# Optimization experiments

Hardware: AMD Instinct MI355X
Metric: run time of the kernel (lower is better)

The kernel has to match this reference:

```python
import jax, jax.numpy as jnp
import numpy as np

B, N, C, P, K = 8, 65536, 96, 96, 512


def _ln(x, g, b, eps=1e-5):
    mu = x.mean(axis=-1, keepdims=True)
    var = ((x - mu) ** 2).mean(axis=-1, keepdims=True)
    return (x - mu) * jax.lax.rsqrt(var + eps) * g + b


def setup_inputs():
    key = jax.random.key(0)
    ks = jax.random.split(key, 8)
    inp = {
        "pts_feat": jax.random.normal(ks[0], (B, N, C), jnp.float32),
        "sp_idx": jax.random.randint(ks[1], (B, N), 0, K, jnp.int64),
        "all_xyz": jax.random.normal(ks[2], (B, N, 3), jnp.float32),
        # pts_proj1: Linear(3,P) -> LN -> ReLU -> Linear(P,P) -> LN
        "W1": jax.random.normal(ks[3], (3, P), jnp.float32) / np.sqrt(3.0),
        "b1": jnp.zeros((P,), jnp.float32),
        "g1": jnp.ones((P,), jnp.float32),
        "be1": jnp.zeros((P,), jnp.float32),
        "W2": jax.random.normal(ks[4], (P, P), jnp.float32) / np.sqrt(P),
        "b2": jnp.zeros((P,), jnp.float32),
        "g2": jnp.ones((P,), jnp.float32),
        "be2": jnp.zeros((P,), jnp.float32),
        # pts_proj2: Linear(2P,P) -> LN -> ReLU -> Linear(P,1,no bias) -> Sigmoid
        "W3": jax.random.normal(ks[5], (2 * P, P), jnp.float32) / np.sqrt(2.0 * P),
        "b3": jnp.zeros((P,), jnp.float32),
        "g3": jnp.ones((P,), jnp.float32),
        "be3": jnp.zeros((P,), jnp.float32),
        "W4": jax.random.normal(ks[6], (P, 1), jnp.float32) / np.sqrt(P),
        "num_sp": K,
    }
    return inp


def reference(pts_feat, sp_idx, all_xyz, W1, b1, g1, be1, W2, b2, g2, be2,
              W3, b3, g3, be3, W4, num_sp):
    Bx, Nx, Cx = pts_feat.shape
    S = Bx * num_sp  # total superpoints across batch (uniform K per batch)
    idx = (sp_idx + jnp.arange(Bx, dtype=sp_idx.dtype)[:, None] * num_sp).reshape(-1)
    xyz = all_xyz.reshape(-1, 3)
    feat = pts_feat.reshape(-1, Cx)

    # scatter_norm: unit-sphere normalize per segment
    mn = jax.ops.segment_min(xyz, idx, num_segments=S)
    mx = jax.ops.segment_max(xyz, idx, num_segments=S)
    cnt = jax.ops.segment_sum(jnp.ones((xyz.shape[0],), xyz.dtype), idx, num_segments=S)
    cnt_c = jnp.maximum(cnt, 1.0)
    center = jax.ops.segment_sum(xyz, idx, num_segments=S) / cnt_c[:, None]
    diam = (mx - mn).max(axis=1)
    pts = (xyz - center[idx]) / (diam[idx][:, None] + 0.01)

    # pts_proj1
    h = _ln(pts @ W1 + b1, g1, be1)
    h = jax.nn.relu(h)
    h = _ln(h @ W2 + b2, g2, be2)

    seg = jax.ops.segment_max(h, idx, num_segments=S)  # (S, P)
    cat = jnp.concatenate([h, seg[idx]], axis=-1)      # (B*N, 2P)

    # pts_proj2
    z = _ln(cat @ W3 + b3, g3, be3)
    z = jax.nn.relu(z)
    w = jax.nn.sigmoid(z @ W4) * 2.0                   # (B*N, 1)

    sp_feat = jax.ops.segment_sum(feat * w, idx, num_segments=S) / cnt_c[:, None] + seg
    return sp_feat.reshape(Bx, num_sp, Cx), w.reshape(Bx, Nx, 1)
```

## Files before the change

kernel.cpp:

```cpp
#include <hip/hip_runtime.h>
#include <cstdint>

#define MM 524288
#define NSEG 4096
#define NWIN2 32768u

#define WS_SCNT   0u
#define WS_CURSOR 4096u
#define WS_OFFS   8192u
#define WS_M1     12288u
#define WS_CENTER 12304u
#define WS_DIAM   24592u
#define WS_SEGF   28688u
#define WS_ZSEG   421904u
#define WS_SORTED 815120u
#define WS_SEG16  1339408u
#define WS_WSRT   1601552u
#define WS_H8     2125840u
#define WS_WMAX   27291664u
#define WS_END    28864528u

typedef __attribute__((ext_vector_type(8))) short short8;
typedef __attribute__((ext_vector_type(4))) float f32x4;

#define WPAD 104

__device__ __forceinline__ unsigned bfr(float x) {
    unsigned u = __float_as_uint(x);
    return (u + 0x7FFFu + ((u >> 16) & 1u)) >> 16;
}
__device__ __forceinline__ float bf2f(unsigned v) {
    return __uint_as_float(v << 16);
}
union U4S8 { uint4 u; short8 s; };

__global__ void __launch_bounds__(256) k0_init(unsigned* __restrict__ ws)
{
    unsigned i = blockIdx.x * 256u + threadIdx.x;
    if (i < 8192u) ws[i] = 0u;
}

__global__ void __launch_bounds__(256) k1_count(
    const int* __restrict__ spidx, unsigned* __restrict__ scnt)
{
    __shared__ unsigned lcnt[512];
    int tid = threadIdx.x;
    for (int j = tid; j < 512; j += 256) lcnt[j] = 0u;
    __syncthreads();
    int base = blockIdx.x * 4096;
    #pragma unroll 4
    for (int it = 0; it < 16; ++it) {
        int p = base + it*256 + tid;
        atomicAdd(&lcnt[spidx[p]], 1u);
    }
    __syncthreads();
    int b = blockIdx.x >> 4;
    for (int j = tid; j < 512; j += 256)
        atomicAdd(&scnt[(b << 9) + j], lcnt[j]);
}

__global__ void __launch_bounds__(1024) k2_scan(
    const unsigned* __restrict__ scnt, unsigned* __restrict__ offs,
    const float* __restrict__ W1, const float* __restrict__ b1, float* __restrict__ m1)
{
    __shared__ unsigned sh[1024];
    int t = threadIdx.x;
    unsigned c0 = scnt[t*4+0], c1 = scnt[t*4+1], c2 = scnt[t*4+2], c3 = scnt[t*4+3];
    unsigned tot = c0 + c1 + c2 + c3;
    sh[t] = tot;
    __syncthreads();
    for (int d = 1; d < 1024; d <<= 1) {
        unsigned v = (t >= d) ? sh[t-d] : 0u;
        __syncthreads();
        sh[t] += v;
        __syncthreads();
    }
    unsigned excl = sh[t] - tot;
    offs[t*4+0] = excl;
    offs[t*4+1] = excl + c0;
    offs[t*4+2] = excl + c0 + c1;
    offs[t*4+3] = excl + c0 + c1 + c2;

    if (t == 0) {
        float Sa=0,Sb=0,Sc=0,Sd=0,Saa=0,Sbb=0,Scc=0,Sdd=0,Sab=0,Sac=0,Sad=0,Sbc=0,Sbd=0,Scd=0;
        #pragma unroll 8
        for (int j = 0; j < 96; ++j) {
            float A = W1[j], B2 = W1[96+j], C2 = W1[192+j], D = b1[j];
            Sa+=A; Sb+=B2; Sc+=C2; Sd+=D;
            Saa=fmaf(A,A,Saa); Sbb=fmaf(B2,B2,Sbb); Scc=fmaf(C2,C2,Scc); Sdd=fmaf(D,D,Sdd);
            Sab=fmaf(A,B2,Sab); Sac=fmaf(A,C2,Sac); Sad=fmaf(A,D,Sad);
            Sbc=fmaf(B2,C2,Sbc); Sbd=fmaf(B2,D,Sbd); Scd=fmaf(C2,D,Scd);
        }
        const float inv = 1.f/96.f;
        float Am=Sa*inv, Bm=Sb*inv, Cm=Sc*inv, Dm=Sd*inv;
        m1[0]=Am; m1[1]=Bm; m1[2]=Cm; m1[3]=Dm;
        m1[4]=Saa*inv-Am*Am; m1[5]=Sbb*inv-Bm*Bm; m1[6]=Scc*inv-Cm*Cm; m1[7]=Sdd*inv-Dm*Dm;
        m1[8]=Sab*inv-Am*Bm; m1[9]=Sac*inv-Am*Cm; m1[10]=Sad*inv-Am*Dm;
        m1[11]=Sbc*inv-Bm*Cm; m1[12]=Sbd*inv-Bm*Dm; m1[13]=Scd*inv-Cm*Dm;
    }
}

__global__ void __launch_bounds__(256) k3_scatter(
    const int* __restrict__ spidx, const unsigned* __restrict__ offs,
    unsigned* __restrict__ cursor, unsigned* __restrict__ sorted,
    unsigned short* __restrict__ seg16)
{
    __shared__ unsigned lcnt[512];
    __shared__ unsigned gbase[512];
    __shared__ unsigned short rank16[4096];
    int tid = threadIdx.x;
    for (int j = tid; j < 512; j += 256) lcnt[j] = 0u;
    __syncthreads();
    int base = blockIdx.x * 4096;
    #pragma unroll 4
    for (int it = 0; it < 16; ++it) {
        int p = base + it*256 + tid;
        unsigned r = atomicAdd(&lcnt[spidx[p]], 1u);
        rank16[it*256 + tid] = (unsigned short)r;
    }
    __syncthreads();
    int b = blockIdx.x >> 4;
    for (int j = tid; j < 512; j += 256)
        gbase[j] = atomicAdd(&cursor[(b << 9) + j], lcnt[j]);
    __syncthreads();
    #pragma unroll 4
    for (int it = 0; it < 16; ++it) {
        int p = base + it*256 + tid;
        int sl = spidx[p];
        int s = (b << 9) + sl;
        unsigned pos = offs[s] + gbase[sl] + (unsigned)rank16[it*256 + tid];
        sorted[pos] = (unsigned)p;
        seg16[pos] = (unsigned short)s;
    }
}

__global__ void __launch_bounds__(128) k3b_stats(
    const float* __restrict__ xyz, const unsigned* __restrict__ sorted,
    const unsigned* __restrict__ offs, const unsigned* __restrict__ scnt,
    float* __restrict__ center, float* __restrict__ diam)
{
    int s = blockIdx.x, tid = threadIdx.x;
    unsigned cnt = scnt[s], off = offs[s];
    float mnx=INFINITY, mny=INFINITY, mnz=INFINITY;
    float mxx=-INFINITY, mxy=-INFINITY, mxz=-INFINITY;
    float smx=0.f, smy=0.f, smz=0.f;
    for (unsigned r = tid; r < cnt; r += 128) {
        unsigned p = sorted[off + r];
        float x = xyz[3*p], y = xyz[3*p+1], z = xyz[3*p+2];
        mnx = fminf(mnx, x); mny = fminf(mny, y); mnz = fminf(mnz, z);
        mxx = fmaxf(mxx, x); mxy = fmaxf(mxy, y); mxz = fmaxf(mxz, z);
        smx += x; smy += y; smz += z;
    }
    #pragma unroll
    for (int m = 1; m < 64; m <<= 1) {
        mnx = fminf(mnx, __shfl_xor(mnx, m)); mny = fminf(mny, __shfl_xor(mny, m));
        mnz = fminf(mnz, __shfl_xor(mnz, m));
        mxx = fmaxf(mxx, __shfl_xor(mxx, m)); mxy = fmaxf(mxy, __shfl_xor(mxy, m));
        mxz = fmaxf(mxz, __shfl_xor(mxz, m));
        smx += __shfl_xor(smx, m); smy += __shfl_xor(smy, m); smz += __shfl_xor(smz, m);
    }
    __shared__ float cw[2][9];
    if ((tid & 63) == 0) {
        int w = tid >> 6;
        cw[w][0]=mnx; cw[w][1]=mny; cw[w][2]=mnz;
        cw[w][3]=mxx; cw[w][4]=mxy; cw[w][5]=mxz;
        cw[w][6]=smx; cw[w][7]=smy; cw[w][8]=smz;
    }
    __syncthreads();
    if (tid == 0) {
        float a0=fminf(cw[0][0],cw[1][0]), a1=fminf(cw[0][1],cw[1][1]), a2=fminf(cw[0][2],cw[1][2]);
        float b0=fmaxf(cw[0][3],cw[1][3]), b1=fmaxf(cw[0][4],cw[1][4]), b2=fmaxf(cw[0][5],cw[1][5]);
        float s0=cw[0][6]+cw[1][6], s1=cw[0][7]+cw[1][7], s2=cw[0][8]+cw[1][8];
        float cc = fmaxf((float)cnt, 1.f);
        center[s*3+0] = s0/cc; center[s*3+1] = s1/cc; center[s*3+2] = s2/cc;
        diam[s] = fmaxf(fmaxf(b0-a0, b1-a1), b2-a2);
    }
}

__global__ void __launch_bounds__(256) kTA(
    const float* __restrict__ xyz,
    const unsigned* __restrict__ sorted,
    const unsigned short* __restrict__ seg16,
    const float* __restrict__ center, const float* __restrict__ diam,
    const float* __restrict__ W1, const float* __restrict__ b1,
    const float* __restrict__ g1, const float* __restrict__ be1,
    const float* __restrict__ m1,
    const float* __restrict__ W2, const float* __restrict__ b2,
    const float* __restrict__ g2, const float* __restrict__ be2,
    uint4* __restrict__ h8)
{
    __shared__ unsigned short wT[96*WPAD];
    __shared__ float pw8[96*8];
    __shared__ float prm[3*96];
    __shared__ float mcl[14];
    int tid = threadIdx.x;
    #pragma unroll 4
    for (int it = 0; it < 36; ++it) {
        int e = it*256 + tid;
        int i = e / 96, j = e - i*96;
        wT[j*WPAD + i] = (unsigned short)bfr(W2[e]);
    }
    if (tid < 96) {
        pw8[tid*8+0] = W1[tid]; pw8[tid*8+1] = W1[96+tid]; pw8[tid*8+2] = W1[192+tid];
        pw8[tid*8+3] = b1[tid]; pw8[tid*8+4] = g1[tid];    pw8[tid*8+5] = be1[tid];
        pw8[tid*8+6] = 0.f;     pw8[tid*8+7] = 0.f;
        prm[tid] = b2[tid]; prm[96+tid] = g2[tid]; prm[192+tid] = be2[tid];
    }
    if (tid < 14) mcl[tid] = m1[tid];
    __syncthreads();

    int lane = tid & 63, w = tid >> 6;
    int pcol = lane & 15, g = lane >> 4;
    size_t slot0 = (size_t)blockIdx.x * 256 + w*64 + pcol;
    const f32x4* pwv = (const f32x4*)pw8;

    #pragma unroll 1
    for (int t = 0; t < 4; ++t) {
        size_t slot = slot0 + (size_t)t * 16;
        unsigned p = sorted[slot];
        int s = seg16[slot];
        float dinv = 1.f / (diam[s] + 0.01f);
        float px = (xyz[3*p+0] - center[3*s+0]) * dinv;
        float py = (xyz[3*p+1] - center[3*s+1]) * dinv;
        float pz = (xyz[3*p+2] - center[3*s+2]) * dinv;

        float mu = fmaf(px, mcl[0], fmaf(py, mcl[1], fmaf(pz, mcl[2], mcl[3])));
        float var = fmaf(px*px, mcl[4], fmaf(py*py, mcl[5], fmaf(pz*pz, mcl[6], mcl[7])));
        var = fmaf(2.f*px*py, mcl[8],  var);
        var = fmaf(2.f*px*pz, mcl[9],  var);
        var = fmaf(2.f*px,    mcl[10], var);
        var = fmaf(2.f*py*pz, mcl[11], var);
        var = fmaf(2.f*py,    mcl[12], var);
        var = fmaf(2.f*pz,    mcl[13], var);
        float rs = rsqrtf(var + 1e-5f);

        f32x4 acc[6];
        #pragma unroll
        for (int nt = 0; nt < 6; ++nt) acc[nt] = (f32x4){0.f,0.f,0.f,0.f};

        #pragma unroll
        for (int ks = 0; ks < 3; ++ks) {
            U4S8 bu;
            unsigned vv[4];
            #pragma unroll
            for (int e2 = 0; e2 < 4; ++e2) {
                int i0 = ks*32 + g*8 + e2*2;
                f32x4 lo0 = pwv[i0*2],     hi0 = pwv[i0*2+1];
                f32x4 lo1 = pwv[(i0+1)*2], hi1 = pwv[(i0+1)*2+1];
                float ta = fmaf(px, lo0[0], fmaf(py, lo0[1], fmaf(pz, lo0[2], lo0[3])));
                ta = fmaxf(fmaf((ta - mu) * rs, hi0[0], hi0[1]), 0.f);
                float tb = fmaf(px, lo1[0], fmaf(py, lo1[1], fmaf(pz, lo1[2], lo1[3])));
                tb = fmaxf(fmaf((tb - mu) * rs, hi1[0], hi1[1]), 0.f);
                vv[e2] = bfr(ta) | (bfr(tb) << 16);
            }
            bu.u.x = vv[0]; bu.u.y = vv[1]; bu.u.z = vv[2]; bu.u.w = vv[3];
            #pragma unroll
            for (int nt = 0; nt < 6; ++nt) {
                const short8 aF = *(const short8*)&wT[(nt*16 + pcol)*WPAD + ks*32 + g*8];
                acc[nt] = __builtin_amdgcn_mfma_f32_16x16x32_bf16(aF, bu.s, acc[nt], 0, 0, 0);
            }
        }

        float sum = 0.f, sq = 0.f;
        #pragma unroll
        for (int nt = 0; nt < 6; ++nt) {
            f32x4 bv = *(const f32x4*)&prm[nt*16 + g*4];
            #pragma unroll
            for (int r = 0; r < 4; ++r) {
                float v = acc[nt][r] + bv[r];
                acc[nt][r] = v;
                sum += v;
                sq = fmaf(v, v, sq);
            }
        }
        sum += __shfl_xor(sum, 16); sum += __shfl_xor(sum, 32);
        sq  += __shfl_xor(sq, 16);  sq  += __shfl_xor(sq, 32);
        float muh = sum * (1.f/96.f);
        float rsh = rsqrtf(sq * (1.f/96.f) - muh*muh + 1e-5f);

        #pragma unroll
        for (int nt = 0; nt < 6; ++nt) {
            f32x4 gv  = *(const f32x4*)&prm[96  + nt*16 + g*4];
            f32x4 bev = *(const f32x4*)&prm[192 + nt*16 + g*4];
            float o0 = fmaf((acc[nt][0]-muh)*rsh, gv[0], bev[0]);
            float o1 = fmaf((acc[nt][1]-muh)*rsh, gv[1], bev[1]);
            float o2 = fmaf((acc[nt][2]-muh)*rsh, gv[2], bev[2]);
            float o3 = fmaf((acc[nt][3]-muh)*rsh, gv[3], bev[3]);
            uint2 st;
            st.x = bfr(o0) | (bfr(o1) << 16);
            st.y = bfr(o2) | (bfr(o3) << 16);
            int j0 = nt*16 + g*4;
            size_t q = (size_t)(nt*2 + (g >> 1));
            *(uint2*)((char*)h8 + (q*MM + slot)*16 + (size_t)(j0 & 7)*2) = st;
        }
    }
}

__global__ void __launch_bounds__(256) kW_winmax(
    const unsigned* __restrict__ h8u32, unsigned* __restrict__ wmax32)
{
    unsigned gw = blockIdx.x * 4u + (threadIdx.x >> 6);
    unsigned lane = threadIdx.x & 63u;
    unsigned base = gw * 4u;
    unsigned q = base >> 15;
    unsigned win0 = base & 32767u;
    size_t qoff = (size_t)q * MM * 4u;
    #pragma unroll
    for (int i = 0; i < 4; ++i) {
        unsigned win = win0 + i;
        unsigned v = h8u32[qoff + (size_t)win * 64u + lane];
        float f0 = bf2f(v & 0xFFFFu);
        float f1 = __uint_as_float(v & 0xFFFF0000u);
        #pragma unroll
        for (int m = 4; m < 64; m <<= 1) {
            f0 = fmaxf(f0, __shfl_xor(f0, m));
            f1 = fmaxf(f1, __shfl_xor(f1, m));
        }
        if (lane < 4) {
            unsigned st = (__float_as_uint(f0) >> 16) | (__float_as_uint(f1) & 0xFFFF0000u);
            wmax32[(size_t)win * 48u + q * 4u + lane] = st;
        }
    }
}

__global__ void __launch_bounds__(128) kZ_seg(
    const unsigned short* __restrict__ wmax16,
    const unsigned short* __restrict__ h8u16,
    const unsigned* __restrict__ offs, const unsigned* __restrict__ scnt,
    const float* __restrict__ W3, const float* __restrict__ b3,
    float* __restrict__ segf, float* __restrict__ zseg)
{
    __shared__ float lseg[96];
    int s = blockIdx.x, tid = threadIdx.x;
    unsigned cnt = scnt[s], off = offs[s];
    if (tid < 96) {
        int q = tid >> 3, e = tid & 7;
        size_t qstr = (size_t)q * MM * 8 + e;
        unsigned a = off, b = off + cnt;
        unsigned af = (a + 15u) & ~15u, bf = b & ~15u;
        float mx = -INFINITY;
        if (af < bf) {
            for (unsigned wn = af >> 4; wn < (bf >> 4); ++wn)
                mx = fmaxf(mx, bf2f(wmax16[(size_t)wn*96 + tid]));
        }
        unsigned h1 = min(af, b);
        for (unsigned sl = a; sl < h1; ++sl)
            mx = fmaxf(mx, bf2f(h8u16[qstr + (size_t)sl*8]));
        unsigned t0 = max(bf, h1);
        for (unsigned sl = t0; sl < b; ++sl)
            mx = fmaxf(mx, bf2f(h8u16[qstr + (size_t)sl*8]));
        segf[(size_t)s*96 + tid] = mx;
        lseg[tid] = mx;
    }
    __syncthreads();
    if (tid < 96) {
        float acc = b3[tid];
        #pragma unroll 4
        for (int i = 0; i < 96; ++i)
            acc = fmaf(lseg[i], W3[(size_t)(96+i)*96 + tid], acc);
        zseg[(size_t)s*96 + tid] = acc;
    }
}

__global__ void __launch_bounds__(256) kC_mfma(
    const uint4* __restrict__ h8, const float* __restrict__ zseg,
    const unsigned short* __restrict__ seg16, const unsigned* __restrict__ sorted,
    const float* __restrict__ W3, const float* __restrict__ g3,
    const float* __restrict__ be3, const float* __restrict__ W4,
    float* __restrict__ w_nat, float* __restrict__ w_srt)
{
    __shared__ unsigned short wT[96*WPAD];
    __shared__ float prm[3*96];
    int tid = threadIdx.x;
    #pragma unroll 4
    for (int it = 0; it < 36; ++it) {
        int e = it*256 + tid;
        int i = e / 96, j = e - i*96;
        wT[j*WPAD + i] = (unsigned short)bfr(W3[e]);
    }
    if (tid < 96) { prm[tid] = g3[tid]; prm[96+tid] = be3[tid]; prm[192+tid] = W4[tid]; }
    __syncthreads();

    int lane = tid & 63, w = tid >> 6;
    int pcol = lane & 15, g = lane >> 4;
    size_t slot0 = (size_t)blockIdx.x * 256 + w*64 + pcol;

    uint4 B0 = h8[(size_t)(0*4+g) * MM + slot0];
    uint4 B1 = h8[(size_t)(1*4+g) * MM + slot0];
    uint4 B2q = h8[(size_t)(2*4+g) * MM + slot0];

    #pragma unroll 1
    for (int t = 0; t < 4; ++t) {
        size_t slot = slot0 + (size_t)t * 16;
        uint4 C0 = B0, C1 = B1, C2 = B2q;
        if (t < 3) {
            size_t sn = slot + 16;
            C0 = h8[(size_t)(0*4+g) * MM + sn];
            C1 = h8[(size_t)(1*4+g) * MM + sn];
            C2 = h8[(size_t)(2*4+g) * MM + sn];
        }
        U4S8 u0, u1, u2; u0.u = B0; u1.u = B1; u2.u = B2q;
        short8 bB[3] = { u0.s, u1.s, u2.s };

        f32x4 acc[6];
        #pragma unroll
        for (int nt = 0; nt < 6; ++nt) acc[nt] = (f32x4){0.f,0.f,0.f,0.f};

        #pragma unroll
        for (int ks = 0; ks < 3; ++ks) {
            #pragma unroll
            for (int nt = 0; nt < 6; ++nt) {
                const short8 aF = *(const short8*)&wT[(nt*16 + pcol)*WPAD + ks*32 + g*8];
                acc[nt] = __builtin_amdgcn_mfma_f32_16x16x32_bf16(aF, bB[ks], acc[nt], 0, 0, 0);
            }
        }

        int s = seg16[slot];
        float sum = 0.f, sq = 0.f;
        #pragma unroll
        for (int nt = 0; nt < 6; ++nt) {
            f32x4 zs = *(const f32x4*)&zseg[(size_t)s*96 + nt*16 + g*4];
            #pragma unroll
            for (int r = 0; r < 4; ++r) {
                float v = acc[nt][r] + zs[r];
                acc[nt][r] = v;
                sum += v;
                sq = fmaf(v, v, sq);
            }
        }
        sum += __shfl_xor(sum, 16); sum += __shfl_xor(sum, 32);
        sq  += __shfl_xor(sq, 16);  sq  += __shfl_xor(sq, 32);
        float mu = sum * (1.f/96.f);
        float rs = rsqrtf(sq * (1.f/96.f) - mu*mu + 1e-5f);

        float tt = 0.f;
        #pragma unroll
        for (int nt = 0; nt < 6; ++nt) {
            f32x4 gv  = *(const f32x4*)&prm[nt*16 + g*4];
            f32x4 bev = *(const f32x4*)&prm[96 + nt*16 + g*4];
            f32x4 w4v = *(const f32x4*)&prm[192 + nt*16 + g*4];
            #pragma unroll
            for (int r = 0; r < 4; ++r) {
                float v = fmaxf(fmaf((acc[nt][r]-mu)*rs, gv[r], bev[r]), 0.f);
                tt = fmaf(v, w4v[r], tt);
            }
        }
        tt += __shfl_xor(tt, 16); tt += __shfl_xor(tt, 32);
        if (lane < 16) {
            float wv = 2.f / (1.f + expf(-tt));
            w_srt[slot] = wv;
            w_nat[sorted[slot]] = wv;
        }
        B0 = C0; B1 = C1; B2q = C2;
    }
}

__global__ void __launch_bounds__(128) kD_pool(
    const float* __restrict__ feat, const float* __restrict__ w_srt,
    const unsigned* __restrict__ sorted, const unsigned* __restrict__ offs,
    const unsigned* __restrict__ scnt, const float* __restrict__ segf,
    float* __restrict__ sp_out)
{
    int s = blockIdx.x;
    int c = threadIdx.x;
    unsigned cnt = scnt[s], off = offs[s];
    float acc = 0.f;
    unsigned r = 0;
    for (; r + 8 <= cnt; r += 8) {
        unsigned pp[8]; float ww[8];
        #pragma unroll
        for (int k = 0; k < 8; ++k) {
            pp[k] = sorted[off + r + k];
            ww[k] = w_srt[off + r + k];
        }
        if (c < 96) {
            #pragma unroll
            for (int k = 0; k < 8; ++k)
                acc = fmaf(feat[(size_t)pp[k]*96 + c], ww[k], acc);
        }
    }
    for (; r < cnt; ++r) {
        unsigned p0 = sorted[off + r];
        float w0 = w_srt[off + r];
        if (c < 96) acc = fmaf(feat[(size_t)p0*96 + c], w0, acc);
    }
    if (c < 96) {
        float cc = fmaxf((float)cnt, 1.f);
        sp_out[(size_t)s*96 + c] = acc / cc + segf[(size_t)s*96 + c];
    }
}

extern "C" void kernel_launch(void* const* d_in, const int* in_sizes, int n_in,
                              void* d_out, int out_size, void* d_ws, size_t ws_size,
                              hipStream_t stream)
{
    const float* pts_feat = (const float*)d_in[0];
    const int*   sp_idx   = (const int*)d_in[1];
    const float* xyz      = (const float*)d_in[2];
    const float* W1  = (const float*)d_in[3];
    const float* b1  = (const float*)d_in[4];
    const float* g1  = (const float*)d_in[5];
    const float* be1 = (const float*)d_in[6];
    const float* W2  = (const float*)d_in[7];
    const float* b2  = (const float*)d_in[8];
    const float* g2  = (const float*)d_in[9];
    const float* be2 = (const float*)d_in[10];
    const float* W3  = (const float*)d_in[11];
    const float* b3  = (const float*)d_in[12];
    const float* g3  = (const float*)d_in[13];
    const float* be3 = (const float*)d_in[14];
    const float* W4  = (const float*)d_in[15];

    float* out = (float*)d_out;
    float* sp_out = out;
    float* w_out  = out + (size_t)NSEG * 96;

    if (ws_size < (size_t)WS_END * 4u) return;

    unsigned* ws32   = (unsigned*)d_ws;
    unsigned* scnt   = ws32 + WS_SCNT;
    unsigned* cursor = ws32 + WS_CURSOR;
    unsigned* offs   = ws32 + WS_OFFS;
    float*    m1     = (float*)(ws32 + WS_M1);
    float*    center = (float*)(ws32 + WS_CENTER);
    float*    diam   = (float*)(ws32 + WS_DIAM);
    float*    segf   = (float*)(ws32 + WS_SEGF);
    float*    zseg   = (float*)(ws32 + WS_ZSEG);
    unsigned* sorted = ws32 + WS_SORTED;
    unsigned short* seg16 = (unsigned short*)(ws32 + WS_SEG16);
    float*    w_srt  = (float*)(ws32 + WS_WSRT);
    uint4*    h8     = (uint4*)(ws32 + WS_H8);
    unsigned* wmax32 = ws32 + WS_WMAX;

    k0_init<<<32, 256, 0, stream>>>(ws32);
    k1_count<<<MM/4096, 256, 0, stream>>>(sp_idx, scnt);
    k2_scan<<<1, 1024, 0, stream>>>(scnt, offs, W1, b1, m1);
    k3_scatter<<<MM/4096, 256, 0, stream>>>(sp_idx, offs, cursor, sorted, seg16);
    k3b_stats<<<NSEG, 128, 0, stream>>>(xyz, sorted, offs, scnt, center, diam);
    kTA<<<MM/256, 256, 0, stream>>>(xyz, sorted, seg16, center, diam,
        W1, b1, g1, be1, m1, W2, b2, g2, be2, h8);
    kW_winmax<<<(NWIN2*12u)/16u, 256, 0, stream>>>((const unsigned*)h8, wmax32);
    kZ_seg<<<NSEG, 128, 0, stream>>>((const unsigned short*)wmax32,
        (const unsigned short*)h8, offs, scnt, W3, b3, segf, zseg);
    kC_mfma<<<MM/256, 256, 0, stream>>>(h8, zseg, seg16, sorted, W3, g3, be3, W4,
        w_out, w_srt);
    kD_pool<<<NSEG, 128, 0, stream>>>(pts_feat, w_srt, sorted, offs, scnt, segf, sp_out);
}
```

Measured before the change: 303.8 us.

## Replace window-max prepass with direct per-segment max over sorted h8 tiles

Drops the kW_winmax kernel and its wmax workspace, which precomputed 16-row window maxima. The per-segment kernel now reads every row of its segment straight from the sorted h8 buffer in 16-row chunks, staged through shared memory, and reduces the max there. This saves a launch and a full pass over h8 plus the wmax writes. In exchange each segment block rereads its whole segment, pays two barriers per chunk, and leaves half of its threads idle during the reduction.

```diff
diff --git a/kernel.cpp b/kernel.cpp
--- a/kernel.cpp
+++ b/kernel.cpp
@@ -3,7 +3,6 @@
 
 #define MM 524288
 #define NSEG 4096
-#define NWIN2 32768u
 
 #define WS_SCNT   0u
 #define WS_CURSOR 4096u
@@ -17,8 +16,7 @@
 #define WS_SEG16  1339408u
 #define WS_WSRT   1601552u
 #define WS_H8     2125840u
-#define WS_WMAX   27291664u
-#define WS_END    28864528u
+#define WS_END    (WS_H8 + 25165824u)
 
 typedef __attribute__((ext_vector_type(8))) short short8;
 typedef __attribute__((ext_vector_type(4))) float f32x4;
@@ -296,62 +294,35 @@
     }
 }
 
-__global__ void __launch_bounds__(256) kW_winmax(
-    const unsigned* __restrict__ h8u32, unsigned* __restrict__ wmax32)
-{
-    unsigned gw = blockIdx.x * 4u + (threadIdx.x >> 6);
-    unsigned lane = threadIdx.x & 63u;
-    unsigned base = gw * 4u;
-    unsigned q = base >> 15;
-    unsigned win0 = base & 32767u;
-    size_t qoff = (size_t)q * MM * 4u;
-    #pragma unroll
-    for (int i = 0; i < 4; ++i) {
-        unsigned win = win0 + i;
-        unsigned v = h8u32[qoff + (size_t)win * 64u + lane];
-        float f0 = bf2f(v & 0xFFFFu);
-        float f1 = __uint_as_float(v & 0xFFFF0000u);
-        #pragma unroll
-        for (int m = 4; m < 64; m <<= 1) {
-            f0 = fmaxf(f0, __shfl_xor(f0, m));
-            f1 = fmaxf(f1, __shfl_xor(f1, m));
-        }
-        if (lane < 4) {
-            unsigned st = (__float_as_uint(f0) >> 16) | (__float_as_uint(f1) & 0xFFFF0000u);
-            wmax32[(size_t)win * 48u + q * 4u + lane] = st;
-        }
-    }
-}
-
-__global__ void __launch_bounds__(128) kZ_seg(
-    const unsigned short* __restrict__ wmax16,
-    const unsigned short* __restrict__ h8u16,
+__global__ void __launch_bounds__(192) kB_seg(
+    const uint4* __restrict__ h8,
     const unsigned* __restrict__ offs, const unsigned* __restrict__ scnt,
     const float* __restrict__ W3, const float* __restrict__ b3,
     float* __restrict__ segf, float* __restrict__ zseg)
 {
+    __shared__ uint4 st[16][13];
     __shared__ float lseg[96];
     int s = blockIdx.x, tid = threadIdx.x;
     unsigned cnt = scnt[s], off = offs[s];
-    if (tid < 96) {
-        int q = tid >> 3, e = tid & 7;
-        size_t qstr = (size_t)q * MM * 8 + e;
-        unsigned a = off, b = off + cnt;
-        unsigned af = (a + 15u) & ~15u, bf = b & ~15u;
-        float mx = -INFINITY;
-        if (af < bf) {
-            for (unsigned wn = af >> 4; wn < (bf >> 4); ++wn)
-                mx = fmaxf(mx, bf2f(wmax16[(size_t)wn*96 + tid]));
-        }
-        unsigned h1 = min(af, b);
-        for (unsigned sl = a; sl < h1; ++sl)
-            mx = fmaxf(mx, bf2f(h8u16[qstr + (size_t)sl*8]));
-        unsigned t0 = max(bf, h1);
-        for (unsigned sl = t0; sl < b; ++sl)
-            mx = fmaxf(mx, bf2f(h8u16[qstr + (size_t)sl*8]));
-        segf[(size_t)s*96 + tid] = mx;
-        lseg[tid] = mx;
-    }
+    int r = tid & 15, q = tid >> 4;
+    float mx = -INFINITY;
+    for (unsigned base = 0; base < cnt; base += 16) {
+        uint4 v = make_uint4(0xFF80FF80u, 0xFF80FF80u, 0xFF80FF80u, 0xFF80FF80u);
+        if (q < 12 && base + (unsigned)r < cnt)
+            v = h8[(size_t)q * MM + off + base + r];
+        if (q < 12) st[r][q] = v;
+        __syncthreads();
+        if (tid < 96) {
+            int qj = tid >> 3, ej = tid & 7;
+            #pragma unroll
+            for (int rr = 0; rr < 16; ++rr) {
+                const unsigned short* hp = (const unsigned short*)&st[rr][qj];
+                mx = fmaxf(mx, bf2f(hp[ej]));
+            }
+        }
+        __syncthreads();
+    }
+    if (tid < 96) { segf[(size_t)s*96 + tid] = mx; lseg[tid] = mx; }
     __syncthreads();
     if (tid < 96) {
         float acc = b3[tid];
@@ -530,7 +501,6 @@
     unsigned short* seg16 = (unsigned short*)(ws32 + WS_SEG16);
     float*    w_srt  = (float*)(ws32 + WS_WSRT);
     uint4*    h8     = (uint4*)(ws32 + WS_H8);
-    unsigned* wmax32 = ws32 + WS_WMAX;
 
     k0_init<<<32, 256, 0, stream>>>(ws32);
     k1_count<<<MM/4096, 256, 0, stream>>>(sp_idx, scnt);
@@ -539,9 +509,7 @@
     k3b_stats<<<NSEG, 128, 0, stream>>>(xyz, sorted, offs, scnt, center, diam);
     kTA<<<MM/256, 256, 0, stream>>>(xyz, sorted, seg16, center, diam,
         W1, b1, g1, be1, m1, W2, b2, g2, be2, h8);
-    kW_winmax<<<(NWIN2*12u)/16u, 256, 0, stream>>>((const unsigned*)h8, wmax32);
-    kZ_seg<<<NSEG, 128, 0, stream>>>((const unsigned short*)wmax32,
-        (const unsigned short*)h8, offs, scnt, W3, b3, segf, zseg);
+    kB_seg<<<NSEG, 192, 0, stream>>>(h8, offs, scnt, W3, b3, segf, zseg);
     kC_mfma<<<MM/256, 256, 0, stream>>>(h8, zseg, seg16, sorted, W3, g3, be3, W4,
         w_out, w_srt);
     kD_pool<<<NSEG, 128, 0, stream>>>(pts_feat, w_srt, sorted, offs, scnt, segf, sp_out);
```

Measured after the change: 275.9 us. 1.1x faster.
